# Optimization experiments

Measured on AMD Instinct MI355X. Metric: run time of the kernel, lower is better.

Reference implementation:

```python
import jax, jax.numpy as jnp
import numpy as np

R = 8          # gate_r
SIGMA = 4.0
PER_SPK_MAX = 32
TOP_M = 64
N_HEADS = 8


def _window_mean(A, spikes, r):
    # A:[B,T], spikes:[B,S] int -> mean of A over [ti-r, ti+r] clipped to [0,T)
    B, T = A.shape
    off = jnp.arange(-r, r + 1)
    t = spikes[:, :, None] + off                      # [B,S,W]
    valid = (t >= 0) & (t < T)
    tc = jnp.clip(t, 0, T - 1)
    vals = A[jnp.arange(B)[:, None, None], tc]        # [B,S,W]
    return (vals * valid).sum(-1) / jnp.maximum(valid.sum(-1), 1)


def setup_inputs() -> dict:
    key = jax.random.key(0)
    ks = jax.random.split(key, 12)
    Kspk, B, T, S0 = 3, 8, 8192, 128
    d_proj = d_c = d_model = 512
    s = 0.02
    return {
        'proj_feats': jax.random.normal(ks[0], (B, T, d_proj), jnp.float32),
        'h_ctc': jax.random.normal(ks[1], (Kspk, B, T, d_c), jnp.float32),
        'A': jax.random.uniform(ks[2], (Kspk, B, T), jnp.float32),
        'spikes': jax.random.randint(ks[3], (Kspk, B, S0), 0, T),
        'W_mem': jax.random.normal(ks[4], (d_proj, d_model), jnp.float32) * s,
        'b_mem': jnp.zeros((d_model,), jnp.float32),
        'W_kv': jax.random.normal(ks[5], (Kspk, d_c, 2 * d_model), jnp.float32) * s,
        'b_kv': jnp.zeros((Kspk, 2 * d_model), jnp.float32),
        'W_q': jax.random.normal(ks[6], (d_model, d_model), jnp.float32) * s,
        'b_q': jnp.zeros((d_model,), jnp.float32),
        'W_qkv': jax.random.normal(ks[7], (d_model, 3 * d_model), jnp.float32) * s,
        'b_qkv': jnp.zeros((3 * d_model,), jnp.float32),
        'W_attn_out': jax.random.normal(ks[8], (d_model, d_model), jnp.float32) * s,
        'b_attn_out': jnp.zeros((d_model,), jnp.float32),
        'W_o': jax.random.normal(ks[9], (d_model, d_model), jnp.float32) * s,
        'b_o': jnp.zeros((d_model,), jnp.float32),
    }


def reference(proj_feats, h_ctc, A, spikes, W_mem, b_mem, W_kv, b_kv,
              W_q, b_q, W_qkv, b_qkv, W_attn_out, b_attn_out, W_o, b_o):
    Kspk, B, T, _ = h_ctc.shape
    d_model = W_mem.shape[1]
    hd = d_model // N_HEADS
    # memory = projected mixed features (K = V = M_mem)
    M = proj_feats @ W_mem + b_mem                                  # [B,T,d]
    Wqh, Wkh, Wvh = jnp.split(W_qkv, 3, axis=1)
    bqh, bkh, bvh = jnp.split(b_qkv, 3)
    k_mem = (M @ Wkh + bkh).reshape(B, T, N_HEADS, hd)
    v_mem = (M @ Wvh + bvh).reshape(B, T, N_HEADS, hd)
    off = jnp.arange(-R, R + 1)
    gauss = jnp.exp(-0.5 * (off / SIGMA) ** 2)                      # [W]
    bidx = jnp.arange(B)[:, None, None]
    tracks = []
    for k in range(Kspk):
        A_k, sp = A[k], spikes[k]
        k_keep = min(PER_SPK_MAX, sp.shape[1], TOP_M)
        # prune spikes by local mean of A (top-k per batch)
        sc = jnp.where((sp >= 0) & (sp < T), _window_mean(A_k, sp, R), -1e9)
        _, top_idx = jax.lax.top_k(sc, k_keep)
        spk = jnp.take_along_axis(sp, top_idx, axis=1)              # [B,S]
        # Gaussian-weighted window pooling around each kept spike
        t = spk[:, :, None] + off                                   # [B,S,W]
        valid = (t >= 0) & (t < T)
        tc = jnp.clip(t, 0, T - 1)
        w = gauss * A_k[bidx, tc] * valid                           # [B,S,W]
        Z = jnp.einsum('bsw,bswd->bsd', w, h_ctc[k][bidx, tc]) / (w.sum(-1, keepdims=True) + 1e-6)
        vmask = ((spk >= 0) & (spk < T)).astype(M.dtype)            # all ones here
        # K_seed = first half of kv_ctc[k](Z); queries
        K_seed = (Z @ W_kv[k] + b_kv[k])[..., :d_model]
        Qk = jnp.tanh(K_seed @ W_q + b_q)                           # [B,S,d]
        # cross-attention (nn.MultiheadAttention, batch_first)
        q = (Qk @ Wqh + bqh).reshape(B, -1, N_HEADS, hd)
        attn = jax.nn.softmax(
            jnp.einsum('bqhd,bthd->bhqt', q, k_mem) / jnp.sqrt(jnp.float32(hd)), axis=-1)
        ctx = jnp.einsum('bhqt,bthd->bqhd', attn, v_mem).reshape(B, -1, d_model)
        fused = (ctx @ W_attn_out + b_attn_out) @ W_o + b_o
        # confidence gate (computed under no_grad in the original)
        conf = jax.lax.stop_gradient(jnp.where(vmask > 0, _window_mean(A_k, spk, R), 0.0))
        gk = jax.nn.sigmoid(2.0 * conf) * vmask
        tracks.append(fused * gk[..., None])
    return jnp.concatenate(tracks, axis=1)                          # [B, K*S, d]
```

## Files before the change

kernel.cpp:

```cpp
#include <hip/hip_runtime.h>
#include <hip/hip_bf16.h>


#define T_LEN 8192
#define DMODEL 512
#define NROWS 768

typedef __hip_bfloat16 bf16;
typedef short s16x8 __attribute__((ext_vector_type(8)));
typedef short s16x4 __attribute__((ext_vector_type(4)));
typedef float f32x4 __attribute__((ext_vector_type(4)));
typedef float f4 __attribute__((ext_vector_type(4)));
typedef float f2 __attribute__((ext_vector_type(2)));
typedef int i32x4 __attribute__((ext_vector_type(4)));

typedef __attribute__((address_space(3))) void* lds_vp;
typedef const __attribute__((address_space(1))) void* gbl_cvp;

__global__ __launch_bounds__(256) void prep_w2t(const float* __restrict__ Wmem,
                                                const float* __restrict__ Wqkv,
                                                bf16* __restrict__ w2t) {
  __shared__ __align__(16) float As[16][68];
  __shared__ __align__(16) float Bs[16][68];
  int tid = threadIdx.x;
  int j0 = blockIdx.x * 64, i0 = blockIdx.y * 64;
  int ty = tid >> 4, tx = tid & 15;
  float c[4][4];
#pragma unroll
  for (int a = 0; a < 4; a++)
#pragma unroll
    for (int b = 0; b < 4; b++) c[a][b] = 0.f;

  for (int l0 = 0; l0 < 512; l0 += 16) {
    __syncthreads();
    {
      int l = tid >> 4, j4 = (tid & 15) * 4;
      f4 v = *(const f4*)&Wqkv[(size_t)(l0 + l) * 1536 + 512 + j0 + j4];
      *(f4*)&As[l][j4] = v;
    }
    {
      int i = tid >> 2, l4 = (tid & 3) * 4;
      f4 v = *(const f4*)&Wmem[(size_t)(i0 + i) * 512 + l0 + l4];
      Bs[l4 + 0][i] = v[0];
      Bs[l4 + 1][i] = v[1];
      Bs[l4 + 2][i] = v[2];
      Bs[l4 + 3][i] = v[3];
    }
    __syncthreads();
#pragma unroll
    for (int l = 0; l < 16; l++) {
      f4 a = *(f4*)&As[l][ty * 4];
      f4 b = *(f4*)&Bs[l][tx * 4];
#pragma unroll
      for (int jj = 0; jj < 4; jj++)
#pragma unroll
        for (int ii = 0; ii < 4; ii++) c[jj][ii] += a[jj] * b[ii];
    }
  }
#pragma unroll
  for (int jj = 0; jj < 4; jj++)
#pragma unroll
    for (int ii = 0; ii < 4; ii++)
      w2t[(size_t)(j0 + ty * 4 + jj) * 512 + i0 + tx * 4 + ii] =
          __float2bfloat16(c[jj][ii]);
}

__global__ __launch_bounds__(256) void bias2_kernel(const float* __restrict__ bmem,
                                                    const float* __restrict__ Wqkv,
                                                    const float* __restrict__ bqkv,
                                                    float* __restrict__ b2) {
  __shared__ float red[4][64];
  int j0 = blockIdx.x * 64;
  int jc = threadIdx.x & 63, lp = threadIdx.x >> 6;
  int j = j0 + jc;
  float acc = 0.f;
  for (int l = lp * 128; l < lp * 128 + 128; l++)
    acc += bmem[l] * Wqkv[(size_t)l * 1536 + 512 + j];
  red[lp][jc] = acc;
  __syncthreads();
  if (threadIdx.x < 64) {
    float s = red[0][jc] + red[1][jc] + red[2][jc] + red[3][jc];
    b2[j0 + jc] = s + bqkv[512 + j0 + jc];
  }
}

__global__ __launch_bounds__(256) void cvt_bf16(const float* __restrict__ x,
                                                bf16* __restrict__ y) {
  int i = blockIdx.x * 256 + threadIdx.x;
  const f4* p = (const f4*)x;
  f4 a = p[(size_t)i * 2], b = p[(size_t)i * 2 + 1];
  __align__(16) bf16 o[8];
  o[0] = __float2bfloat16(a[0]);
  o[1] = __float2bfloat16(a[1]);
  o[2] = __float2bfloat16(a[2]);
  o[3] = __float2bfloat16(a[3]);
  o[4] = __float2bfloat16(b[0]);
  o[5] = __float2bfloat16(b[1]);
  o[6] = __float2bfloat16(b[2]);
  o[7] = __float2bfloat16(b[3]);
  ((f4*)y)[i] = *(f4*)o;
}

__global__ __launch_bounds__(256) void kv_gemm(const bf16* __restrict__ A,
                                               const bf16* __restrict__ Bt,
                                               const float* __restrict__ bias,
                                               bf16* __restrict__ C) {
  __shared__ __align__(16) char sm[16384];
  bf16* As = (bf16*)sm;
  bf16* Bs = (bf16*)(sm + 8192);
  int tid = threadIdx.x;
  int lane = tid & 63, wave = tid >> 6;
  int wm = wave & 1, wn = wave >> 1;
  int m0 = blockIdx.y * 128, n0 = blockIdx.x * 128;
  int l15 = lane & 15, g = lane >> 4;
  f32x4 acc[4][4];
#pragma unroll
  for (int mi = 0; mi < 4; mi++)
#pragma unroll
    for (int ni = 0; ni < 4; ni++) acc[mi][ni] = (f32x4){0.f, 0.f, 0.f, 0.f};

  int arow = tid >> 2, akq = (tid & 3) * 8;
  for (int k0 = 0; k0 < 512; k0 += 32) {
    __syncthreads();
#pragma unroll
    for (int i = 0; i < 2; i++) {
      const bf16* ga = &A[(size_t)(m0 + i * 64 + arow) * 512 + k0 + akq];
      const bf16* gb = &Bt[(size_t)(n0 + i * 64 + arow) * 512 + k0 + akq];
      __builtin_amdgcn_global_load_lds((gbl_cvp)ga,
                                       (lds_vp)(sm + (i * 256 + wave * 64) * 16),
                                       16, 0, 0);
      __builtin_amdgcn_global_load_lds((gbl_cvp)gb,
                                       (lds_vp)(sm + 8192 + (i * 256 + wave * 64) * 16),
                                       16, 0, 0);
    }
    __syncthreads();
    s16x8 af[4], bfr[4];
#pragma unroll
    for (int mi = 0; mi < 4; mi++)
      af[mi] = *(s16x8*)&As[(wm * 64 + mi * 16 + l15) * 32 + g * 8];
#pragma unroll
    for (int ni = 0; ni < 4; ni++)
      bfr[ni] = *(s16x8*)&Bs[(wn * 64 + ni * 16 + l15) * 32 + g * 8];
#pragma unroll
    for (int mi = 0; mi < 4; mi++)
#pragma unroll
      for (int ni = 0; ni < 4; ni++)
        acc[mi][ni] = __builtin_amdgcn_mfma_f32_16x16x32_bf16(bfr[ni], af[mi],
                                                              acc[mi][ni], 0, 0, 0);
  }

  short* ep = (short*)sm;
  int band = wm * 16 + l15;
#pragma unroll
  for (int mi = 0; mi < 4; mi++) {
    __syncthreads();
#pragma unroll
    for (int ni = 0; ni < 4; ni++) {
      int c0 = wn * 64 + ni * 16 + g * 4;
      f4 bv = *(const f4*)&bias[n0 + c0];
      f32x4 v = acc[mi][ni];
      __align__(8) bf16 pk[4];
#pragma unroll
      for (int r = 0; r < 4; r++) pk[r] = __float2bfloat16(v[r] + bv[r]);
      *(s16x4*)&ep[band * 136 + c0] = *(s16x4*)pk;
    }
    __syncthreads();
#pragma unroll
    for (int it = 0; it < 2; it++) {
      int cidx = it * 256 + tid;
      int brow = cidx >> 4, ch = cidx & 15;
      s16x8 val = *(s16x8*)&ep[brow * 136 + ch * 8];
      int row = m0 + (brow >> 4) * 64 + mi * 16 + (brow & 15);
      *(s16x8*)&C[(size_t)row * 1024 + n0 + ch * 8] = val;
    }
  }
}

__global__ __launch_bounds__(128) void topk_kernel(const float* __restrict__ A,
                                                   const int* __restrict__ spikes,
                                                   int* __restrict__ spk_out,
                                                   float* __restrict__ w_out,
                                                   float* __restrict__ winv_out,
                                                   float* __restrict__ gk_out) {
  int kb = blockIdx.x;
  int i = threadIdx.x;
  const float* Ab = A + (size_t)kb * T_LEN;
  __shared__ float s_sc[128];
  __shared__ int s_sp[128];
  __shared__ int s_sel[32];
  int t0 = spikes[kb * 128 + i];
  s_sp[i] = t0;
  float sum = 0.f;
  int cnt = 0;
#pragma unroll
  for (int o = -8; o <= 8; o++) {
    int t = t0 + o;
    if (t >= 0 && t < T_LEN) { sum += Ab[t]; cnt++; }
  }
  float sc = (t0 >= 0 && t0 < T_LEN) ? (sum / (float)max(cnt, 1)) : -1e9f;
  s_sc[i] = sc;
  __syncthreads();
  float sci = s_sc[i];
  int rank = 0;
  for (int j = 0; j < 128; j++) {
    float scj = s_sc[j];
    if (scj > sci || (scj == sci && j < i)) rank++;
  }
  if (rank < 32) s_sel[rank] = i;
  __syncthreads();
  if (i < 32) {
    int sel = s_sel[i];
    int spkv = s_sp[sel];
    float conf = s_sc[sel];
    int r = kb * 32 + i;
    spk_out[r] = spkv;
    bool vmask = (spkv >= 0 && spkv < T_LEN);
    float wsum = 0.f;
#pragma unroll
    for (int o = 0; o < 17; o++) {
      int t = spkv + o - 8;
      bool v = vmask && (t >= 0) && (t < T_LEN);
      int tc = min(max(t, 0), T_LEN - 1);
      float off = (float)(o - 8) * 0.25f;
      float g = expf(-0.5f * off * off);
      float wv = v ? g * Ab[tc] : 0.f;
      wsum += wv;
      w_out[r * 17 + o] = wv;
    }
    winv_out[r] = 1.f / (wsum + 1e-6f);
    gk_out[r] = vmask ? (1.f / (1.f + expf(-2.f * conf))) : 0.f;
  }
}

__global__ __launch_bounds__(256) void z_gather(const float* __restrict__ hctc,
                                                const int* __restrict__ spk,
                                                const float* __restrict__ warr,
                                                const float* __restrict__ winv,
                                                float* __restrict__ Z) {
  int r = blockIdx.x;
  int tid = threadIdx.x;
  int kb = r >> 5;
  const float* h = hctc + (size_t)kb * T_LEN * DMODEL;
  int sp = spk[r];
  float wi = winv[r];
  float acc0 = 0.f, acc1 = 0.f;
#pragma unroll
  for (int o = 0; o < 17; o++) {
    float wv = warr[r * 17 + o];
    int t = min(max(sp + o - 8, 0), T_LEN - 1);
    const float* hp = h + (size_t)t * DMODEL;
    acc0 += wv * hp[tid];
    acc1 += wv * hp[tid + 256];
  }
  Z[(size_t)r * DMODEL + tid] = acc0 * wi;
  Z[(size_t)r * DMODEL + tid + 256] = acc1 * wi;
}

__global__ __launch_bounds__(256) void seed_chain(
    const float* __restrict__ Z, const float* __restrict__ Wkv,
    const float* __restrict__ bkv, const float* __restrict__ Wq,
    const float* __restrict__ bq, const float* __restrict__ Wqkv,
    const float* __restrict__ bqkv, float* __restrict__ qout) {
  __shared__ float Zs[8][512];
  __shared__ float T1[8][512];
  __shared__ float T2[8][512];
  int tid = threadIdx.x;
  int r0 = blockIdx.x * 8;
  int k = r0 >> 8;
  for (int ii = 0; ii < 16; ii++) {
    int idx = tid + ii * 256;
    ((float*)Zs)[idx] = Z[(size_t)r0 * 512 + idx];
  }
  __syncthreads();
  int c0 = tid, c1 = tid + 256;
  {
    const float* W = Wkv + (size_t)k * 512 * 1024;
    float a0[8], a1[8];
#pragma unroll
    for (int i = 0; i < 8; i++) { a0[i] = 0.f; a1[i] = 0.f; }
#pragma unroll 4
    for (int l = 0; l < 512; l++) {
      float w0 = W[(size_t)l * 1024 + c0];
      float w1 = W[(size_t)l * 1024 + c1];
#pragma unroll
      for (int i = 0; i < 8; i++) {
        float z = Zs[i][l];
        a0[i] += z * w0;
        a1[i] += z * w1;
      }
    }
    float bb0 = bkv[k * 1024 + c0], bb1 = bkv[k * 1024 + c1];
#pragma unroll
    for (int i = 0; i < 8; i++) {
      T1[i][c0] = a0[i] + bb0;
      T1[i][c1] = a1[i] + bb1;
    }
  }
  __syncthreads();
  {
    float a0[8], a1[8];
#pragma unroll
    for (int i = 0; i < 8; i++) { a0[i] = 0.f; a1[i] = 0.f; }
#pragma unroll 4
    for (int l = 0; l < 512; l++) {
      float w0 = Wq[(size_t)l * 512 + c0];
      float w1 = Wq[(size_t)l * 512 + c1];
#pragma unroll
      for (int i = 0; i < 8; i++) {
        float z = T1[i][l];
        a0[i] += z * w0;
        a1[i] += z * w1;
      }
    }
    float bb0 = bq[c0], bb1 = bq[c1];
#pragma unroll
    for (int i = 0; i < 8; i++) {
      T2[i][c0] = tanhf(a0[i] + bb0);
      T2[i][c1] = tanhf(a1[i] + bb1);
    }
  }
  __syncthreads();
  {
    float a0[8], a1[8];
#pragma unroll
    for (int i = 0; i < 8; i++) { a0[i] = 0.f; a1[i] = 0.f; }
#pragma unroll 4
    for (int l = 0; l < 512; l++) {
      float w0 = Wqkv[(size_t)l * 1536 + c0];
      float w1 = Wqkv[(size_t)l * 1536 + c1];
#pragma unroll
      for (int i = 0; i < 8; i++) {
        float z = T2[i][l];
        a0[i] += z * w0;
        a1[i] += z * w1;
      }
    }
    float bb0 = bqkv[c0], bb1 = bqkv[c1];
#pragma unroll
    for (int i = 0; i < 8; i++) {
      qout[(size_t)(r0 + i) * 512 + c0] = a0[i] + bb0;
      qout[(size_t)(r0 + i) * 512 + c1] = a1[i] + bb1;
    }
  }
}


static __device__ __forceinline__ unsigned bf16rne(float f) {
  unsigned x = __builtin_bit_cast(unsigned, f);
  return (x + 0x7fffu + ((x >> 16) & 1u)) >> 16;
}
static __device__ __forceinline__ float bfval(unsigned u) {
  return __builtin_bit_cast(float, u << 16);
}
static __device__ __forceinline__ void hilo(float x, unsigned& h, unsigned& l) {
  h = bf16rne(x);
  l = bf16rne(x - bfval(h));
}

__global__ __launch_bounds__(256) void attn_kernel(const bf16* __restrict__ kv,
                                                   const float* __restrict__ qws,
                                                   float* __restrict__ pm,
                                                   float* __restrict__ pl,
                                                   float* __restrict__ pu) {
  __shared__ __align__(16) char smem[40960];
  short* Vts = (short*)smem;
  short* Qls = (short*)(smem + 16384);
  float* ctxc = (float*)smem;
  float* cmS = (float*)(smem + 34816);
  float* clS = (float*)(smem + 35328);

  int tid = threadIdx.x;
  int w = tid >> 6, lane = tid & 63;
  int l15 = lane & 15, g = lane >> 4;
  int bx = blockIdx.x;
  int c = bx & 7, h = (bx >> 3) & 7, b = bx >> 6;
  const short* kvS = (const short*)kv;
  int hoff = h * 64;
  int rowK = b * T_LEN + c * 1024 + w * 256;

#pragma unroll
  for (int p = 0; p < 3; p++) {
    int slot = p * 4 + (tid >> 6);
    int kk = slot >> 2, qt = (slot >> 1) & 1, ds = slot & 1;
    int ln = tid & 63;
    int sl15 = ln & 15, sg = ln >> 4;
    const float* qp = qws + (size_t)((kk * 8 + b) * 32 + qt * 16 + sl15) * 512 +
                      hoff + ds * 32 + sg * 8;
    f4 x = *(const f4*)qp;
    f4 y = *(const f4*)(qp + 4);
    x *= 0.125f;
    y *= 0.125f;
    s16x8 hi, lo;
#pragma unroll
    for (int j = 0; j < 4; j++) {
      unsigned hb, lb;
      hilo(x[j], hb, lb);
      hi[j] = (short)hb;
      lo[j] = (short)lb;
      hilo(y[j], hb, lb);
      hi[4 + j] = (short)hb;
      lo[4 + j] = (short)lb;
    }
    *(s16x8*)&Qls[((slot * 2 + 0) * 64 + ln) * 8] = hi;
    *(s16x8*)&Qls[((slot * 2 + 1) * 64 + ln) * 8] = lo;
  }
  __syncthreads();

  float mq[3][2];
  float lsm[3][2];
  f32x4 ctx[3][4][2];
#pragma unroll
  for (int kk = 0; kk < 3; kk++)
#pragma unroll
    for (int qt = 0; qt < 2; qt++) {
      mq[kk][qt] = -3.0e38f;
      lsm[kk][qt] = 0.f;
    }
#pragma unroll
  for (int kk = 0; kk < 3; kk++)
#pragma unroll
    for (int dt = 0; dt < 4; dt++)
#pragma unroll
      for (int qt = 0; qt < 2; qt++) ctx[kk][dt][qt] = (f32x4){0.f, 0.f, 0.f, 0.f};

  int a0 = (l15 + (((2 * g) & 3) << 4)) << 2;
  int a1 = a0 + 64;

  for (int st = 0; st < 8; st++) {
    int tbase = st * 32;
    s16x8 kf[2][2];
#pragma unroll
    for (int mt = 0; mt < 2; mt++) {
      size_t krow = (size_t)(rowK + tbase + mt * 16 + l15) * 1024 + hoff;
#pragma unroll
      for (int ds = 0; ds < 2; ds++)
        kf[mt][ds] = *(const s16x8*)(kvS + krow + ds * 32 + g * 8);
    }
    {
      s16x8 vv[4];
#pragma unroll
      for (int i = 0; i < 4; i++)
        vv[i] = *(const s16x8*)(kvS +
                                (size_t)(rowK + tbase + i * 8 + (lane >> 3)) * 1024 +
                                512 + hoff + (lane & 7) * 8);
#pragma unroll
      for (int i = 0; i < 4; i++) {
        int tk = i * 8 + (lane >> 3);
        int dbase = (lane & 7) * 8;
#pragma unroll
        for (int j = 0; j < 8; j++) {
          int d = dbase + j;
          Vts[w * 2048 + d * 32 + (tk & 7) + ((i ^ ((d >> 3) & 3)) << 3)] = vv[i][j];
        }
      }
    }
    s16x8 vfr[4];
#pragma unroll
    for (int dt = 0; dt < 4; dt++) {
      int d = dt * 16 + l15;
      vfr[dt] = *(const s16x8*)&Vts[w * 2048 + d * 32 + ((g ^ ((d >> 3) & 3)) << 3)];
    }
#pragma unroll
    for (int kk = 0; kk < 3; kk++) {
      s16x8 qf[2][2][2];
#pragma unroll
      for (int qt = 0; qt < 2; qt++)
#pragma unroll
        for (int ds = 0; ds < 2; ds++)
#pragma unroll
          for (int hl = 0; hl < 2; hl++)
            qf[qt][ds][hl] =
                *(const s16x8*)&Qls[(((kk * 4 + qt * 2 + ds) * 2 + hl) * 64 + lane) * 8];
      f32x4 sa[2][2];
#pragma unroll
      for (int mt = 0; mt < 2; mt++)
#pragma unroll
        for (int qt = 0; qt < 2; qt++) {
          f32x4 acc = (f32x4){0.f, 0.f, 0.f, 0.f};
          acc = __builtin_amdgcn_mfma_f32_16x16x32_bf16(kf[mt][0], qf[qt][0][0], acc, 0, 0, 0);
          acc = __builtin_amdgcn_mfma_f32_16x16x32_bf16(kf[mt][0], qf[qt][0][1], acc, 0, 0, 0);
          acc = __builtin_amdgcn_mfma_f32_16x16x32_bf16(kf[mt][1], qf[qt][1][0], acc, 0, 0, 0);
          acc = __builtin_amdgcn_mfma_f32_16x16x32_bf16(kf[mt][1], qf[qt][1][1], acc, 0, 0, 0);
          sa[mt][qt] = acc;
        }
#pragma unroll
      for (int qt = 0; qt < 2; qt++) {
        f32x4 s0 = sa[0][qt], s1 = sa[1][qt];
        float tm = fmaxf(fmaxf(fmaxf(s0[0], s0[1]), fmaxf(s0[2], s0[3])),
                         fmaxf(fmaxf(s1[0], s1[1]), fmaxf(s1[2], s1[3])));
        tm = fmaxf(tm, __shfl_xor(tm, 16, 64));
        tm = fmaxf(tm, __shfl_xor(tm, 32, 64));
        float mn = fmaxf(mq[kk][qt], tm);
        float p0[4], p1[4];
        float ps = 0.f;
#pragma unroll
        for (int j = 0; j < 4; j++) {
          p0[j] = __expf(s0[j] - mn);
          p1[j] = __expf(s1[j] - mn);
          ps += p0[j] + p1[j];
        }
        ps += __shfl_xor(ps, 16, 64);
        ps += __shfl_xor(ps, 32, 64);
        float sc = __expf(mq[kk][qt] - mn);
        lsm[kk][qt] = lsm[kk][qt] * sc + ps;
        mq[kk][qt] = mn;
#pragma unroll
        for (int dt = 0; dt < 4; dt++) ctx[kk][dt][qt] *= sc;
        unsigned hh[8], ll[8];
#pragma unroll
        for (int j = 0; j < 4; j++) {
          hilo(p0[j], hh[j], ll[j]);
          hilo(p1[j], hh[4 + j], ll[4 + j]);
        }
        unsigned dh0 = hh[0] | (hh[1] << 16), dh1 = hh[2] | (hh[3] << 16);
        unsigned dh2 = hh[4] | (hh[5] << 16), dh3 = hh[6] | (hh[7] << 16);
        unsigned dl0 = ll[0] | (ll[1] << 16), dl1 = ll[2] | (ll[3] << 16);
        unsigned dl2 = ll[4] | (ll[5] << 16), dl3 = ll[6] | (ll[7] << 16);
        int x0 = __builtin_amdgcn_ds_bpermute(a0, (int)dh0);
        int x1 = __builtin_amdgcn_ds_bpermute(a0, (int)dh1);
        int x2 = __builtin_amdgcn_ds_bpermute(a0, (int)dh2);
        int x3 = __builtin_amdgcn_ds_bpermute(a0, (int)dh3);
        int y0 = __builtin_amdgcn_ds_bpermute(a1, (int)dh0);
        int y1 = __builtin_amdgcn_ds_bpermute(a1, (int)dh1);
        int y2 = __builtin_amdgcn_ds_bpermute(a1, (int)dh2);
        int y3 = __builtin_amdgcn_ds_bpermute(a1, (int)dh3);
        i32x4 fh;
        if (g < 2)
          fh = (i32x4){x0, x1, y0, y1};
        else
          fh = (i32x4){x2, x3, y2, y3};
        x0 = __builtin_amdgcn_ds_bpermute(a0, (int)dl0);
        x1 = __builtin_amdgcn_ds_bpermute(a0, (int)dl1);
        x2 = __builtin_amdgcn_ds_bpermute(a0, (int)dl2);
        x3 = __builtin_amdgcn_ds_bpermute(a0, (int)dl3);
        y0 = __builtin_amdgcn_ds_bpermute(a1, (int)dl0);
        y1 = __builtin_amdgcn_ds_bpermute(a1, (int)dl1);
        y2 = __builtin_amdgcn_ds_bpermute(a1, (int)dl2);
        y3 = __builtin_amdgcn_ds_bpermute(a1, (int)dl3);
        i32x4 fl;
        if (g < 2)
          fl = (i32x4){x0, x1, y0, y1};
        else
          fl = (i32x4){x2, x3, y2, y3};
        s16x8 pfh = __builtin_bit_cast(s16x8, fh);
        s16x8 pfl = __builtin_bit_cast(s16x8, fl);
#pragma unroll
        for (int dt = 0; dt < 4; dt++) {
          ctx[kk][dt][qt] =
              __builtin_amdgcn_mfma_f32_16x16x32_bf16(vfr[dt], pfh, ctx[kk][dt][qt], 0, 0, 0);
          ctx[kk][dt][qt] =
              __builtin_amdgcn_mfma_f32_16x16x32_bf16(vfr[dt], pfl, ctx[kk][dt][qt], 0, 0, 0);
        }
      }
    }
  }

#pragma unroll
  for (int kk = 0; kk < 3; kk++) {
    __syncthreads();
    if (g == 0) {
#pragma unroll
      for (int qt = 0; qt < 2; qt++) {
        cmS[w * 32 + qt * 16 + l15] = mq[kk][qt];
        clS[w * 32 + qt * 16 + l15] = lsm[kk][qt];
      }
    }
#pragma unroll
    for (int dt = 0; dt < 4; dt++)
#pragma unroll
      for (int qt = 0; qt < 2; qt++) {
        f32x4 v = ctx[kk][dt][qt];
        int q = qt * 16 + l15;
        int dd = dt * 16 + g * 4;
#pragma unroll
        for (int r = 0; r < 4; r++) ctxc[(w * 32 + q) * 68 + dd + r] = v[r];
      }
    __syncthreads();
    {
      int q = tid >> 3, dg = tid & 7;
      float m0 = cmS[q], m1 = cmS[32 + q], m2 = cmS[64 + q], m3 = cmS[96 + q];
      float ms = fmaxf(fmaxf(m0, m1), fmaxf(m2, m3));
      float e0 = __expf(m0 - ms), e1 = __expf(m1 - ms);
      float e2 = __expf(m2 - ms), e3 = __expf(m3 - ms);
      float ls = e0 * clS[q] + e1 * clS[32 + q] + e2 * clS[64 + q] + e3 * clS[96 + q];
      int pbase = (((kk * 8 + b) * 8 + h) * 8 + c) * 32;
      size_t urow = (size_t)(pbase + q) * 64 + dg * 8;
#pragma unroll
      for (int half = 0; half < 2; half++) {
        int d0 = dg * 8 + half * 4;
        f4 acc = e0 * *(const f4*)&ctxc[q * 68 + d0] +
                 e1 * *(const f4*)&ctxc[(32 + q) * 68 + d0] +
                 e2 * *(const f4*)&ctxc[(64 + q) * 68 + d0] +
                 e3 * *(const f4*)&ctxc[(96 + q) * 68 + d0];
        *(f4*)&pu[urow + half * 4] = acc;
      }
      if (dg == 0) {
        pm[pbase + q] = ms;
        pl[pbase + q] = ls;
      }
    }
  }
}

__global__ __launch_bounds__(256) void out_chain(
    const float* __restrict__ pm, const float* __restrict__ pl,
    const float* __restrict__ pu, const float* __restrict__ Watt,
    const float* __restrict__ batt, const float* __restrict__ Wo,
    const float* __restrict__ bo, const float* __restrict__ gk,
    float* __restrict__ out) {
  __shared__ float Cs[8][512];
  __shared__ float T1[8][512];
  int tid = threadIdx.x;
  int r0 = blockIdx.x * 8;
  {
    int ri = tid >> 5, hh = (tid >> 2) & 7, dq = tid & 3;
    int d0 = dq * 16;
    int r = r0 + ri;
    int k = r >> 8, b = (r >> 5) & 7, s = r & 31;
    int pb0 = ((((k * 8 + b) * 8 + hh) * 8) * 32) + s;
    float mstar = -3.0e38f;
#pragma unroll
    for (int cc = 0; cc < 8; cc++) mstar = fmaxf(mstar, pm[pb0 + cc * 32]);
    float ls = 0.f;
    f4 us[4];
#pragma unroll
    for (int t4 = 0; t4 < 4; t4++) us[t4] = (f4){0.f, 0.f, 0.f, 0.f};
#pragma unroll
    for (int cc = 0; cc < 8; cc++) {
      int pidx = pb0 + cc * 32;
      float wv = __expf(pm[pidx] - mstar);
      ls += wv * pl[pidx];
      const f4* up = (const f4*)&pu[(size_t)pidx * 64 + d0];
#pragma unroll
      for (int t4 = 0; t4 < 4; t4++) us[t4] += up[t4] * wv;
    }
    float inv = 1.f / ls;
#pragma unroll
    for (int t4 = 0; t4 < 4; t4++)
#pragma unroll
      for (int j = 0; j < 4; j++) Cs[ri][hh * 64 + d0 + t4 * 4 + j] = us[t4][j] * inv;
  }
  __syncthreads();
  int c0 = tid, c1 = tid + 256;
  {
    float a0[8], a1[8];
#pragma unroll
    for (int i = 0; i < 8; i++) { a0[i] = 0.f; a1[i] = 0.f; }
#pragma unroll 4
    for (int l = 0; l < 512; l++) {
      float w0 = Watt[(size_t)l * 512 + c0];
      float w1 = Watt[(size_t)l * 512 + c1];
#pragma unroll
      for (int i = 0; i < 8; i++) {
        float z = Cs[i][l];
        a0[i] += z * w0;
        a1[i] += z * w1;
      }
    }
    float bb0 = batt[c0], bb1 = batt[c1];
#pragma unroll
    for (int i = 0; i < 8; i++) {
      T1[i][c0] = a0[i] + bb0;
      T1[i][c1] = a1[i] + bb1;
    }
  }
  __syncthreads();
  {
    float a0[8], a1[8];
#pragma unroll
    for (int i = 0; i < 8; i++) { a0[i] = 0.f; a1[i] = 0.f; }
#pragma unroll 4
    for (int l = 0; l < 512; l++) {
      float w0 = Wo[(size_t)l * 512 + c0];
      float w1 = Wo[(size_t)l * 512 + c1];
#pragma unroll
      for (int i = 0; i < 8; i++) {
        float z = T1[i][l];
        a0[i] += z * w0;
        a1[i] += z * w1;
      }
    }
    float bb0 = bo[c0], bb1 = bo[c1];
#pragma unroll
    for (int i = 0; i < 8; i++) {
      int r = r0 + i;
      int k = r >> 8, b = (r >> 5) & 7, s = r & 31;
      float g = gk[r];
      size_t orow = (size_t)(b * 96 + k * 32 + s) * 512;
      out[orow + c0] = (a0[i] + bb0) * g;
      out[orow + c1] = (a1[i] + bb1) * g;
    }
  }
}

extern "C" void kernel_launch(void* const* d_in, const int* in_sizes, int n_in,
                              void* d_out, int out_size, void* d_ws, size_t ws_size,
                              hipStream_t stream) {
  const float* proj = (const float*)d_in[0];
  const float* hctc = (const float*)d_in[1];
  const float* A = (const float*)d_in[2];
  const int* spikes = (const int*)d_in[3];
  const float* Wmem = (const float*)d_in[4];
  const float* bmem = (const float*)d_in[5];
  const float* Wkv = (const float*)d_in[6];
  const float* bkv = (const float*)d_in[7];
  const float* Wq = (const float*)d_in[8];
  const float* bq = (const float*)d_in[9];
  const float* Wqkv = (const float*)d_in[10];
  const float* bqkv = (const float*)d_in[11];
  const float* Watt = (const float*)d_in[12];
  const float* batt = (const float*)d_in[13];
  const float* Wo = (const float*)d_in[14];
  const float* bo = (const float*)d_in[15];
  float* out = (float*)d_out;
  (void)in_sizes; (void)n_in; (void)out_size; (void)ws_size;

  char* w = (char*)d_ws;
  bf16* projb = (bf16*)(w + 0);
  bf16* kvb   = (bf16*)(w + 67108864);
  bf16* w2t   = (bf16*)(w + 201326592);
  float* b2   = (float*)(w + 202375168);
  int* spk    = (int*)(w + 202379264);
  float* warr = (float*)(w + 202382336);
  float* winv = (float*)(w + 202434560);
  float* gk   = (float*)(w + 202437632);
  float* Zb   = (float*)(w + 202440704);
  float* qws  = (float*)(w + 204013568);
  float* pm   = (float*)(w + 205586432);
  float* pl   = (float*)(w + 205783040);
  float* pu   = (float*)(w + 205979648);

  prep_w2t<<<dim3(16, 8), 256, 0, stream>>>(Wmem, Wqkv, w2t);
  bias2_kernel<<<16, 256, 0, stream>>>(bmem, Wqkv, bqkv, b2);
  cvt_bf16<<<16384, 256, 0, stream>>>(proj, projb);
  kv_gemm<<<dim3(8, 512), 256, 0, stream>>>(projb, w2t, b2, kvb);
  topk_kernel<<<24, 128, 0, stream>>>(A, spikes, spk, warr, winv, gk);
  z_gather<<<768, 256, 0, stream>>>(hctc, spk, warr, winv, Zb);
  seed_chain<<<96, 256, 0, stream>>>(Zb, Wkv, bkv, Wq, bq, Wqkv, bqkv, qws);
  attn_kernel<<<512, 256, 0, stream>>>(kvb, qws, pm, pl, pu);
  out_chain<<<96, 256, 0, stream>>>(pm, pl, pu, Watt, batt, Wo, bo, gk, out);
}
```

Before: 1.125 ms.

## Move seed and output GEMM chains to MFMA with split-bf16 precision

Replaces the fp32 SIMT GEMM chains in seed_chain and out_chain with MFMA kernels (16 rows per block, 8 waves). Precision is kept close to fp32 by splitting each operand into hi/lo bf16 parts and issuing three MFMAs per product. A new prep_wt kernel transposes the five weight matrices into hi/lo bf16 copies, placed in the workspace region that held projb once kv_gemm has consumed it. This targets the scalar FMA and weight-load cost of the small chained GEMMs, at the price of an extra prep pass, triple MFMA work and half as many blocks.

Measured after the change: 958.1 us. -14.8%, faster.

```diff
diff --git a/kernel.cpp b/kernel.cpp
--- a/kernel.cpp
+++ b/kernel.cpp
@@ -16,6 +16,18 @@
 
 typedef __attribute__((address_space(3))) void* lds_vp;
 typedef const __attribute__((address_space(1))) void* gbl_cvp;
+
+static __device__ __forceinline__ unsigned bf16rne(float f) {
+  unsigned x = __builtin_bit_cast(unsigned, f);
+  return (x + 0x7fffu + ((x >> 16) & 1u)) >> 16;
+}
+static __device__ __forceinline__ float bfval(unsigned u) {
+  return __builtin_bit_cast(float, u << 16);
+}
+static __device__ __forceinline__ void hilo(float x, unsigned& h, unsigned& l) {
+  h = bf16rne(x);
+  l = bf16rne(x - bfval(h));
+}
 
 __global__ __launch_bounds__(256) void prep_w2t(const float* __restrict__ Wmem,
                                                 const float* __restrict__ Wqkv,
@@ -84,6 +96,42 @@
   }
 }
 
+__global__ __launch_bounds__(256) void prep_wt(const float* __restrict__ Wkv,
+                                               const float* __restrict__ Wq,
+                                               const float* __restrict__ Wqkv,
+                                               const float* __restrict__ Watt,
+                                               const float* __restrict__ Wo,
+                                               short* __restrict__ wt_hi,
+                                               short* __restrict__ wt_lo) {
+  __shared__ float Ls[64][65];
+  int tid = threadIdx.x;
+  int bx = blockIdx.x, by = blockIdx.y, bz = blockIdx.z;
+  const float* src;
+  int ld;
+  if (bz < 3) { src = Wkv + (size_t)bz * 512 * 1024; ld = 1024; }
+  else if (bz == 3) { src = Wq; ld = 512; }
+  else if (bz == 4) { src = Wqkv; ld = 1536; }
+  else if (bz == 5) { src = Watt; ld = 512; }
+  else { src = Wo; ld = 512; }
+  int t63 = tid & 63, t4 = tid >> 6;
+#pragma unroll
+  for (int p = 0; p < 16; p++) {
+    int row = p * 4 + t4;
+    Ls[row][t63] = src[(size_t)(by * 64 + row) * ld + bx * 64 + t63];
+  }
+  __syncthreads();
+#pragma unroll
+  for (int p = 0; p < 16; p++) {
+    int cc = p * 4 + t4;
+    float v = Ls[t63][cc];
+    unsigned h, l;
+    hilo(v, h, l);
+    size_t idx = (size_t)(bz * 512 + bx * 64 + cc) * 512 + by * 64 + t63;
+    wt_hi[idx] = (short)h;
+    wt_lo[idx] = (short)l;
+  }
+}
+
 __global__ __launch_bounds__(256) void cvt_bf16(const float* __restrict__ x,
                                                 bf16* __restrict__ y) {
   int i = blockIdx.x * 256 + threadIdx.x;
@@ -256,105 +304,85 @@
   Z[(size_t)r * DMODEL + tid + 256] = acc1 * wi;
 }
 
-__global__ __launch_bounds__(256) void seed_chain(
-    const float* __restrict__ Z, const float* __restrict__ Wkv,
-    const float* __restrict__ bkv, const float* __restrict__ Wq,
-    const float* __restrict__ bq, const float* __restrict__ Wqkv,
-    const float* __restrict__ bqkv, float* __restrict__ qout) {
-  __shared__ float Zs[8][512];
-  __shared__ float T1[8][512];
-  __shared__ float T2[8][512];
+__global__ __launch_bounds__(512) void seed_mfma(
+    const float* __restrict__ Z, const short* __restrict__ wt_hi,
+    const short* __restrict__ wt_lo, const float* __restrict__ bkv,
+    const float* __restrict__ bq, const float* __restrict__ bqkv,
+    float* __restrict__ qout) {
+  __shared__ short cb[4][16][520];
   int tid = threadIdx.x;
-  int r0 = blockIdx.x * 8;
-  int k = r0 >> 8;
-  for (int ii = 0; ii < 16; ii++) {
-    int idx = tid + ii * 256;
-    ((float*)Zs)[idx] = Z[(size_t)r0 * 512 + idx];
+  int rb = blockIdx.x * 16;
+  int trk = rb >> 8;
+  int lane = tid & 63, wave = tid >> 6;
+  int l15 = lane & 15, g = lane >> 4;
+  int wbase = wave * 64;
+
+#pragma unroll
+  for (int i = 0; i < 16; i++) {
+    int idx = i * 512 + tid;
+    int row = idx >> 9, col = idx & 511;
+    float v = Z[(size_t)rb * 512 + idx];
+    unsigned h, l;
+    hilo(v, h, l);
+    cb[0][row][col] = (short)h;
+    cb[1][row][col] = (short)l;
   }
   __syncthreads();
-  int c0 = tid, c1 = tid + 256;
-  {
-    const float* W = Wkv + (size_t)k * 512 * 1024;
-    float a0[8], a1[8];
-#pragma unroll
-    for (int i = 0; i < 8; i++) { a0[i] = 0.f; a1[i] = 0.f; }
-#pragma unroll 4
-    for (int l = 0; l < 512; l++) {
-      float w0 = W[(size_t)l * 1024 + c0];
-      float w1 = W[(size_t)l * 1024 + c1];
-#pragma unroll
-      for (int i = 0; i < 8; i++) {
-        float z = Zs[i][l];
-        a0[i] += z * w0;
-        a1[i] += z * w1;
-      }
-    }
-    float bb0 = bkv[k * 1024 + c0], bb1 = bkv[k * 1024 + c1];
-#pragma unroll
-    for (int i = 0; i < 8; i++) {
-      T1[i][c0] = a0[i] + bb0;
-      T1[i][c1] = a1[i] + bb1;
-    }
-  }
-  __syncthreads();
-  {
-    float a0[8], a1[8];
-#pragma unroll
-    for (int i = 0; i < 8; i++) { a0[i] = 0.f; a1[i] = 0.f; }
-#pragma unroll 4
-    for (int l = 0; l < 512; l++) {
-      float w0 = Wq[(size_t)l * 512 + c0];
-      float w1 = Wq[(size_t)l * 512 + c1];
-#pragma unroll
-      for (int i = 0; i < 8; i++) {
-        float z = T1[i][l];
-        a0[i] += z * w0;
-        a1[i] += z * w1;
-      }
-    }
-    float bb0 = bq[c0], bb1 = bq[c1];
-#pragma unroll
-    for (int i = 0; i < 8; i++) {
-      T2[i][c0] = tanhf(a0[i] + bb0);
-      T2[i][c1] = tanhf(a1[i] + bb1);
-    }
-  }
-  __syncthreads();
-  {
-    float a0[8], a1[8];
-#pragma unroll
-    for (int i = 0; i < 8; i++) { a0[i] = 0.f; a1[i] = 0.f; }
-#pragma unroll 4
-    for (int l = 0; l < 512; l++) {
-      float w0 = Wqkv[(size_t)l * 1536 + c0];
-      float w1 = Wqkv[(size_t)l * 1536 + c1];
-#pragma unroll
-      for (int i = 0; i < 8; i++) {
-        float z = T2[i][l];
-        a0[i] += z * w0;
-        a1[i] += z * w1;
-      }
-    }
-    float bb0 = bqkv[c0], bb1 = bqkv[c1];
-#pragma unroll
-    for (int i = 0; i < 8; i++) {
-      qout[(size_t)(r0 + i) * 512 + c0] = a0[i] + bb0;
-      qout[(size_t)(r0 + i) * 512 + c1] = a1[i] + bb1;
-    }
-  }
-}
-
-
-static __device__ __forceinline__ unsigned bf16rne(float f) {
-  unsigned x = __builtin_bit_cast(unsigned, f);
-  return (x + 0x7fffu + ((x >> 16) & 1u)) >> 16;
-}
-static __device__ __forceinline__ float bfval(unsigned u) {
-  return __builtin_bit_cast(float, u << 16);
-}
-static __device__ __forceinline__ void hilo(float x, unsigned& h, unsigned& l) {
-  h = bf16rne(x);
-  l = bf16rne(x - bfval(h));
+
+#pragma unroll
+  for (int stage = 0; stage < 3; stage++) {
+    int sh = (stage & 1) ? 2 : 0;
+    int dh = (stage & 1) ? 0 : 2;
+    int job = (stage == 0) ? trk : (stage == 1 ? 3 : 4);
+    const float* bias = (stage == 0) ? (bkv + trk * 1024) : (stage == 1 ? bq : bqkv);
+    f32x4 acc[4];
+#pragma unroll
+    for (int nt = 0; nt < 4; nt++) acc[nt] = (f32x4){0.f, 0.f, 0.f, 0.f};
+    for (int k0 = 0; k0 < 512; k0 += 32) {
+      s16x8 ah = *(const s16x8*)&cb[sh][l15][k0 + g * 8];
+      s16x8 al = *(const s16x8*)&cb[sh + 1][l15][k0 + g * 8];
+#pragma unroll
+      for (int nt = 0; nt < 4; nt++) {
+        size_t wrow = (size_t)(job * 512 + wbase + nt * 16 + l15) * 512 + k0 + g * 8;
+        s16x8 wh = *(const s16x8*)&wt_hi[wrow];
+        s16x8 wl = *(const s16x8*)&wt_lo[wrow];
+        acc[nt] = __builtin_amdgcn_mfma_f32_16x16x32_bf16(wh, ah, acc[nt], 0, 0, 0);
+        acc[nt] = __builtin_amdgcn_mfma_f32_16x16x32_bf16(wh, al, acc[nt], 0, 0, 0);
+        acc[nt] = __builtin_amdgcn_mfma_f32_16x16x32_bf16(wl, ah, acc[nt], 0, 0, 0);
+      }
+    }
+    if (stage < 2) {
+      __syncthreads();
+#pragma unroll
+      for (int nt = 0; nt < 4; nt++) {
+        int co0 = wbase + nt * 16 + g * 4;
+        f4 bb = *(const f4*)&bias[co0];
+        s16x4 h4, l4;
+#pragma unroll
+        for (int r = 0; r < 4; r++) {
+          float v = acc[nt][r] + bb[r];
+          if (stage == 1) v = tanhf(v);
+          unsigned h, l;
+          hilo(v, h, l);
+          h4[r] = (short)h;
+          l4[r] = (short)l;
+        }
+        *(s16x4*)&cb[dh][l15][co0] = h4;
+        *(s16x4*)&cb[dh + 1][l15][co0] = l4;
+      }
+      __syncthreads();
+    } else {
+#pragma unroll
+      for (int nt = 0; nt < 4; nt++) {
+        int co0 = wbase + nt * 16 + g * 4;
+        f4 bb = *(const f4*)&bias[co0];
+        f4 v;
+#pragma unroll
+        for (int r = 0; r < 4; r++) v[r] = acc[nt][r] + bb[r];
+        *(f4*)&qout[(size_t)(rb + l15) * 512 + co0] = v;
+      }
+    }
+  }
 }
 
 __global__ __launch_bounds__(256) void attn_kernel(const bf16* __restrict__ kv,
@@ -602,22 +630,26 @@
   }
 }
 
-__global__ __launch_bounds__(256) void out_chain(
+__global__ __launch_bounds__(512) void out_mfma(
     const float* __restrict__ pm, const float* __restrict__ pl,
-    const float* __restrict__ pu, const float* __restrict__ Watt,
-    const float* __restrict__ batt, const float* __restrict__ Wo,
+    const float* __restrict__ pu, const short* __restrict__ wt_hi,
+    const short* __restrict__ wt_lo, const float* __restrict__ batt,
     const float* __restrict__ bo, const float* __restrict__ gk,
     float* __restrict__ out) {
-  __shared__ float Cs[8][512];
-  __shared__ float T1[8][512];
+  __shared__ short cb[4][16][520];
   int tid = threadIdx.x;
-  int r0 = blockIdx.x * 8;
+  int rb = blockIdx.x * 16;
+  int lane = tid & 63, wave = tid >> 6;
+  int l15 = lane & 15, g = lane >> 4;
+  int wbase = wave * 64;
+
   {
-    int ri = tid >> 5, hh = (tid >> 2) & 7, dq = tid & 3;
+    int ri = tid >> 5, t32 = tid & 31;
+    int hh = t32 >> 2, dq = t32 & 3;
     int d0 = dq * 16;
-    int r = r0 + ri;
-    int k = r >> 8, b = (r >> 5) & 7, s = r & 31;
-    int pb0 = ((((k * 8 + b) * 8 + hh) * 8) * 32) + s;
+    int r = rb + ri;
+    int kk = r >> 8, b = (r >> 5) & 7, s = r & 31;
+    int pb0 = ((((kk * 8 + b) * 8 + hh) * 8) * 32) + s;
     float mstar = -3.0e38f;
 #pragma unroll
     for (int cc = 0; cc < 8; cc++) mstar = fmaxf(mstar, pm[pb0 + cc * 32]);
@@ -638,57 +670,83 @@
 #pragma unroll
     for (int t4 = 0; t4 < 4; t4++)
 #pragma unroll
-      for (int j = 0; j < 4; j++) Cs[ri][hh * 64 + d0 + t4 * 4 + j] = us[t4][j] * inv;
+      for (int j = 0; j < 4; j++) {
+        float v = us[t4][j] * inv;
+        unsigned h, l;
+        hilo(v, h, l);
+        int col = hh * 64 + d0 + t4 * 4 + j;
+        cb[0][ri][col] = (short)h;
+        cb[1][ri][col] = (short)l;
+      }
   }
   __syncthreads();
-  int c0 = tid, c1 = tid + 256;
+
   {
-    float a0[8], a1[8];
-#pragma unroll
-    for (int i = 0; i < 8; i++) { a0[i] = 0.f; a1[i] = 0.f; }
-#pragma unroll 4
-    for (int l = 0; l < 512; l++) {
-      float w0 = Watt[(size_t)l * 512 + c0];
-      float w1 = Watt[(size_t)l * 512 + c1];
-#pragma unroll
-      for (int i = 0; i < 8; i++) {
-        float z = Cs[i][l];
-        a0[i] += z * w0;
-        a1[i] += z * w1;
-      }
-    }
-    float bb0 = batt[c0], bb1 = batt[c1];
-#pragma unroll
-    for (int i = 0; i < 8; i++) {
-      T1[i][c0] = a0[i] + bb0;
-      T1[i][c1] = a1[i] + bb1;
-    }
-  }
-  __syncthreads();
+    f32x4 acc[4];
+#pragma unroll
+    for (int nt = 0; nt < 4; nt++) acc[nt] = (f32x4){0.f, 0.f, 0.f, 0.f};
+    for (int k0 = 0; k0 < 512; k0 += 32) {
+      s16x8 ah = *(const s16x8*)&cb[0][l15][k0 + g * 8];
+      s16x8 al = *(const s16x8*)&cb[1][l15][k0 + g * 8];
+#pragma unroll
+      for (int nt = 0; nt < 4; nt++) {
+        size_t wrow = (size_t)(5 * 512 + wbase + nt * 16 + l15) * 512 + k0 + g * 8;
+        s16x8 wh = *(const s16x8*)&wt_hi[wrow];
+        s16x8 wl = *(const s16x8*)&wt_lo[wrow];
+        acc[nt] = __builtin_amdgcn_mfma_f32_16x16x32_bf16(wh, ah, acc[nt], 0, 0, 0);
+        acc[nt] = __builtin_amdgcn_mfma_f32_16x16x32_bf16(wh, al, acc[nt], 0, 0, 0);
+        acc[nt] = __builtin_amdgcn_mfma_f32_16x16x32_bf16(wl, ah, acc[nt], 0, 0, 0);
+      }
+    }
+    __syncthreads();
+#pragma unroll
+    for (int nt = 0; nt < 4; nt++) {
+      int co0 = wbase + nt * 16 + g * 4;
+      f4 bb = *(const f4*)&batt[co0];
+      s16x4 h4, l4;
+#pragma unroll
+      for (int r = 0; r < 4; r++) {
+        float v = acc[nt][r] + bb[r];
+        unsigned h, l;
+        hilo(v, h, l);
+        h4[r] = (short)h;
+        l4[r] = (short)l;
+      }
+      *(s16x4*)&cb[2][l15][co0] = h4;
+      *(s16x4*)&cb[3][l15][co0] = l4;
+    }
+    __syncthreads();
+  }
+
   {
-    float a0[8], a1[8];
-#pragma unroll
-    for (int i = 0; i < 8; i++) { a0[i] = 0.f; a1[i] = 0.f; }
-#pragma unroll 4
-    for (int l = 0; l < 512; l++) {
-      float w0 = Wo[(size_t)l * 512 + c0];
-      float w1 = Wo[(size_t)l * 512 + c1];
-#pragma unroll
-      for (int i = 0; i < 8; i++) {
-        float z = T1[i][l];
-        a0[i] += z * w0;
-        a1[i] += z * w1;
-      }
-    }
-    float bb0 = bo[c0], bb1 = bo[c1];
-#pragma unroll
-    for (int i = 0; i < 8; i++) {
-      int r = r0 + i;
-      int k = r >> 8, b = (r >> 5) & 7, s = r & 31;
-      float g = gk[r];
-      size_t orow = (size_t)(b * 96 + k * 32 + s) * 512;
-      out[orow + c0] = (a0[i] + bb0) * g;
-      out[orow + c1] = (a1[i] + bb1) * g;
+    f32x4 acc[4];
+#pragma unroll
+    for (int nt = 0; nt < 4; nt++) acc[nt] = (f32x4){0.f, 0.f, 0.f, 0.f};
+    for (int k0 = 0; k0 < 512; k0 += 32) {
+      s16x8 ah = *(const s16x8*)&cb[2][l15][k0 + g * 8];
+      s16x8 al = *(const s16x8*)&cb[3][l15][k0 + g * 8];
+#pragma unroll
+      for (int nt = 0; nt < 4; nt++) {
+        size_t wrow = (size_t)(6 * 512 + wbase + nt * 16 + l15) * 512 + k0 + g * 8;
+        s16x8 wh = *(const s16x8*)&wt_hi[wrow];
+        s16x8 wl = *(const s16x8*)&wt_lo[wrow];
+        acc[nt] = __builtin_amdgcn_mfma_f32_16x16x32_bf16(wh, ah, acc[nt], 0, 0, 0);
+        acc[nt] = __builtin_amdgcn_mfma_f32_16x16x32_bf16(wh, al, acc[nt], 0, 0, 0);
+        acc[nt] = __builtin_amdgcn_mfma_f32_16x16x32_bf16(wl, ah, acc[nt], 0, 0, 0);
+      }
+    }
+    int r = rb + l15;
+    int kk = r >> 8, b = (r >> 5) & 7, s = r & 31;
+    float gv = gk[r];
+    size_t orow = (size_t)(b * 96 + kk * 32 + s) * 512;
+#pragma unroll
+    for (int nt = 0; nt < 4; nt++) {
+      int co0 = wbase + nt * 16 + g * 4;
+      f4 bb = *(const f4*)&bo[co0];
+      f4 v;
+#pragma unroll
+      for (int r4 = 0; r4 < 4; r4++) v[r4] = (acc[nt][r4] + bb[r4]) * gv;
+      *(f4*)&out[orow + co0] = v;
     }
   }
 }
@@ -729,14 +787,17 @@
   float* pm   = (float*)(w + 205586432);
   float* pl   = (float*)(w + 205783040);
   float* pu   = (float*)(w + 205979648);
+  short* wtHi = (short*)(w + 0);
+  short* wtLo = (short*)(w + 3670016);
 
   prep_w2t<<<dim3(16, 8), 256, 0, stream>>>(Wmem, Wqkv, w2t);
   bias2_kernel<<<16, 256, 0, stream>>>(bmem, Wqkv, bqkv, b2);
   cvt_bf16<<<16384, 256, 0, stream>>>(proj, projb);
   kv_gemm<<<dim3(8, 512), 256, 0, stream>>>(projb, w2t, b2, kvb);
+  prep_wt<<<dim3(8, 8, 7), 256, 0, stream>>>(Wkv, Wq, Wqkv, Watt, Wo, wtHi, wtLo);
   topk_kernel<<<24, 128, 0, stream>>>(A, spikes, spk, warr, winv, gk);
   z_gather<<<768, 256, 0, stream>>>(hctc, spk, warr, winv, Zb);
-  seed_chain<<<96, 256, 0, stream>>>(Zb, Wkv, bkv, Wq, bq, Wqkv, bqkv, qws);
+  seed_mfma<<<48, 512, 0, stream>>>(Zb, wtHi, wtLo, bkv, bq, bqkv, qws);
   attn_kernel<<<512, 256, 0, stream>>>(kvb, qws, pm, pl, pu);
-  out_chain<<<96, 256, 0, stream>>>(pm, pl, pu, Watt, batt, Wo, bo, gk, out);
-}
+  out_mfma<<<48, 512, 0, stream>>>(pm, pl, pu, wtHi, wtLo, batt, bo, gk, out);
+}
```
